# Kernel tuning notes

Hardware: AMD Instinct MI355X
Metric: run time of the kernel (lower is better)

The kernel has to match this reference:

```python
import jax, jax.numpy as jnp
import numpy as np

N = 8192      # active sparse voxels
C = 768       # model_channels
H = 12        # heads
DH = 64       # head dim
NB = 12       # blocks
WS = 8        # window size
RES = 64      # voxel grid resolution
NG = 32       # gaussians per voxel
OUT_CH = 448  # 96+96+96+128+32


def _radical_inverse(base, n):
    inv, f = 0.0, 1.0 / base
    while n > 0:
        inv += f * (n % base)
        n //= base
        f /= base
    return inv


def _hammersley(num):
    return np.array([[i / num, _radical_inverse(2, i), _radical_inverse(3, i)]
                     for i in range(num)], dtype=np.float32)


def _windows(coords, shift):
    # swin partition: window id of each voxel after shifting coords
    wc = (coords.astype(np.int64) + shift) // WS
    G = (RES + shift) // WS + 1
    wid = (wc[:, 0] * G + wc[:, 1]) * G + wc[:, 2]
    uniq, vwin, counts = np.unique(wid, return_inverse=True, return_counts=True)
    nw, cap, n = len(uniq), int(counts.max()), len(wid)
    order = np.argsort(wid, kind='stable')
    starts = np.concatenate([[0], np.cumsum(counts)[:-1]])
    slot_sorted = np.arange(n) - starts[vwin[order]]
    vslot = np.empty(n, dtype=np.int64)
    vslot[order] = slot_sorted
    idx = np.full((nw, cap), n, dtype=np.int32)  # n = padding row
    idx[vwin, vslot] = np.arange(n)
    mask = idx < n
    return (jnp.asarray(idx), jnp.asarray(mask),
            jnp.asarray(vwin.astype(np.int32)), jnp.asarray(vslot.astype(np.int32)))


def setup_inputs() -> dict:
    rng = np.random.RandomState(0)
    coords = rng.randint(0, RES, size=(N, 3)).astype(np.int32)
    feats = rng.randn(N, 8).astype(np.float32)
    idx0, mask0, vwin0, vslot0 = _windows(coords, 0)          # even blocks
    idx1, mask1, vwin1, vslot1 = _windows(coords, WS // 2)    # odd blocks (shifted)
    s = 0.02
    def w(*shape):
        return jnp.asarray((rng.randn(*shape) * s).astype(np.float32))
    perturb = _hammersley(NG) * 2.0 - 1.0
    perturb = np.arctanh(perturb / 1.5).astype(np.float32)  # voxel_size=1.5
    return dict(
        feats=jnp.asarray(feats), coords=jnp.asarray(coords),
        in_w=w(8, C), in_b=jnp.zeros((C,), jnp.float32),
        qkv_w=w(NB, C, 3 * C), qkv_b=jnp.zeros((NB, 3 * C), jnp.float32),
        proj_w=w(NB, C, C), proj_b=jnp.zeros((NB, C), jnp.float32),
        mlp_w1=w(NB, C, 4 * C), mlp_b1=jnp.zeros((NB, 4 * C), jnp.float32),
        mlp_w2=w(NB, 4 * C, C), mlp_b2=jnp.zeros((NB, C), jnp.float32),
        out_w=w(C, OUT_CH), out_b=jnp.zeros((OUT_CH,), jnp.float32),
        perturb=jnp.asarray(perturb),
        idx0=idx0, mask0=mask0, vwin0=vwin0, vslot0=vslot0,
        idx1=idx1, mask1=mask1, vwin1=vwin1, vslot1=vslot1,
    )


def _ln(x, eps):
    mu = jnp.mean(x, -1, keepdims=True)
    xc = x - mu
    var = jnp.mean(xc * xc, -1, keepdims=True)
    return xc * jax.lax.rsqrt(var + eps)


def _pos_embed(coords):
    freq_dim = C // 3 // 2  # 128
    freqs = 1.0 / (10000.0 ** (jnp.arange(freq_dim, dtype=jnp.float32) / freq_dim))
    phase = coords.astype(jnp.float32)[..., None] * freqs          # [N,3,128]
    emb = jnp.concatenate([jnp.sin(phase), jnp.cos(phase)], -1)    # [N,3,256]
    return emb.reshape(coords.shape[0], C)


def _win_attn(q, k, v, idx, mask):
    zpad = jnp.zeros((1,) + q.shape[1:], q.dtype)
    qw = jnp.concatenate([q, zpad], 0)[idx]   # [nw,cap,H,DH]
    kw = jnp.concatenate([k, zpad], 0)[idx]
    vw = jnp.concatenate([v, zpad], 0)[idx]
    scores = jnp.einsum('wihd,wjhd->whij', qw, kw) / np.float32(np.sqrt(DH))
    scores = jnp.where(mask[:, None, None, :], scores, jnp.float32(-1e9))
    attn = jax.nn.softmax(scores, axis=-1)
    return jnp.einsum('whij,wjhd->wihd', attn, vw)   # [nw,cap,H,DH]


def _forward(feats, coords, in_w, in_b, qkv_w, qkv_b, proj_w, proj_b,
             mlp_w1, mlp_b1, mlp_w2, mlp_b2, out_w, out_b, perturb,
             idx0, mask0, vwin0, vslot0, idx1, mask1, vwin1, vslot1):
    cfgs = [(idx0, mask0, vwin0, vslot0), (idx1, mask1, vwin1, vslot1)]
    n = feats.shape[0]
    h = feats @ in_w + in_b + _pos_embed(coords)
    for i in range(NB):
        idx, mask, vwin, vslot = cfgs[i % 2]
        qkv = (_ln(h, 1e-6) @ qkv_w[i] + qkv_b[i]).reshape(n, 3, H, DH)
        ow = _win_attn(qkv[:, 0], qkv[:, 1], qkv[:, 2], idx, mask)
        o = ow[vwin, vslot].reshape(n, C)
        h = h + (o @ proj_w[i] + proj_b[i])
        hid = jax.nn.gelu(_ln(h, 1e-6) @ mlp_w1[i] + mlp_b1[i], approximate=False)
        h = h + (hid @ mlp_w2[i] + mlp_b2[i])
    out = _ln(h, 1e-5) @ out_w + out_b   # F.layer_norm default eps
    # to_representation
    xyz = (coords.astype(jnp.float32) + 0.5) / RES                   # [N,3]
    off = out[:, :96].reshape(n, NG, 3)                               # lr=1.0
    off = jnp.tanh(off + perturb) / RES * 0.5 * 1.5                   # voxel_size=1.5
    g_xyz = (xyz[:, None, :] + off).reshape(n * NG, 3)
    g_dc = out[:, 96:192].reshape(n * NG, 3)
    g_scal = out[:, 192:288].reshape(n * NG, 3)
    g_rot = out[:, 288:416].reshape(n * NG, 4) * 0.1                  # lr=0.1
    g_opa = out[:, 416:448].reshape(n * NG, 1)
    return jnp.concatenate([g_xyz, g_dc, g_scal, g_rot, g_opa], -1)   # [N*32,14]


def reference(feats, coords, in_w, in_b, qkv_w, qkv_b, proj_w, proj_b,
              mlp_w1, mlp_b1, mlp_w2, mlp_b2, out_w, out_b, perturb,
              idx0, mask0, vwin0, vslot0, idx1, mask1, vwin1, vslot1):
    return _forward(feats, coords, in_w, in_b, qkv_w, qkv_b, proj_w, proj_b,
                    mlp_w1, mlp_b1, mlp_w2, mlp_b2, out_w, out_b, perturb,
                    idx0, mask0, vwin0, vslot0, idx1, mask1, vwin1, vslot1)
```

## Files before the change

### kernel.cpp

```cpp
#include <hip/hip_runtime.h>
#include <math.h>

#define NVOX 8192
#define CCH 768
#define NH 12
#define DH 64
#define NBLK 12
#define NG 32
#define OUT_CH 448
#define OUT_PAD 512
#define CAP 48
#define APITCH 72

typedef __attribute__((ext_vector_type(8))) short v8s;
typedef __attribute__((ext_vector_type(4))) float v4f;

__device__ __forceinline__ unsigned short f2bf(float f) {
  unsigned u = __builtin_bit_cast(unsigned, f);
  u += 0x7fffu + ((u >> 16) & 1u);
  return (unsigned short)(u >> 16);
}
__device__ __forceinline__ float bf2f(unsigned short b) {
  return __builtin_bit_cast(float, (unsigned)b << 16);
}

__device__ __forceinline__ void async16(const void* g, void* l) {
  __builtin_amdgcn_global_load_lds(
      (const __attribute__((address_space(1))) unsigned int*)g,
      (__attribute__((address_space(3))) unsigned int*)l, 16, 0, 0);
}

__global__ __launch_bounds__(256) void cap_kernel(const int* __restrict__ a,
                                                  const int* __restrict__ b,
                                                  int n, int* __restrict__ caps) {
  __shared__ int s0[256], s1[256];
  int m0 = 0, m1 = 0;
  for (int i = threadIdx.x; i < n; i += 256) {
    m0 = max(m0, a[i]);
    m1 = max(m1, b[i]);
  }
  s0[threadIdx.x] = m0;
  s1[threadIdx.x] = m1;
  __syncthreads();
  for (int st = 128; st > 0; st >>= 1) {
    if (threadIdx.x < st) {
      s0[threadIdx.x] = max(s0[threadIdx.x], s0[threadIdx.x + st]);
      s1[threadIdx.x] = max(s1[threadIdx.x], s1[threadIdx.x + st]);
    }
    __syncthreads();
  }
  if (threadIdx.x == 0) {
    caps[0] = s0[0] + 1;
    caps[1] = s1[0] + 1;
  }
}

__global__ __launch_bounds__(256) void embed_kernel(const float* __restrict__ feats,
                                                    const int* __restrict__ coords,
                                                    const float* __restrict__ in_w,
                                                    const float* __restrict__ in_b,
                                                    float* __restrict__ h) {
  int id = blockIdx.x * 256 + threadIdx.x;
  if (id >= NVOX * CCH) return;
  int n = id / CCH, c = id - n * CCH;
  float acc = in_b[c];
#pragma unroll
  for (int k = 0; k < 8; ++k) acc += feats[n * 8 + k] * in_w[k * CCH + c];
  int axis = c / 256;
  int r = c - axis * 256;
  int f = r & 127;
  float freq = __expf(-(float)f * (9.210340371976184f / 128.0f));
  float phase = (float)coords[n * 3 + axis] * freq;
  acc += (r < 128) ? __sinf(phase) : __cosf(phase);
  h[id] = acc;
}

__global__ __launch_bounds__(256) void ln_kernel(const float* __restrict__ x,
                                                 unsigned short* __restrict__ y,
                                                 float eps) {
  int row = blockIdx.x;
  const float* xr = x + (size_t)row * CCH;
  float v[3];
  float s = 0.f, s2 = 0.f;
#pragma unroll
  for (int j = 0; j < 3; ++j) {
    v[j] = xr[threadIdx.x + j * 256];
    s += v[j];
    s2 += v[j] * v[j];
  }
#pragma unroll
  for (int off = 32; off >= 1; off >>= 1) {
    s += __shfl_xor(s, off, 64);
    s2 += __shfl_xor(s2, off, 64);
  }
  __shared__ float ss[4], ss2[4];
  int wave = threadIdx.x >> 6, lane = threadIdx.x & 63;
  if (lane == 0) { ss[wave] = s; ss2[wave] = s2; }
  __syncthreads();
  s = ss[0] + ss[1] + ss[2] + ss[3];
  s2 = ss2[0] + ss2[1] + ss2[2] + ss2[3];
  float mu = s * (1.0f / CCH);
  float var = s2 * (1.0f / CCH) - mu * mu;
  float rr = rsqrtf(var + eps);
  unsigned short* yr = y + (size_t)row * CCH;
#pragma unroll
  for (int j = 0; j < 3; ++j) yr[threadIdx.x + j * 256] = f2bf((v[j] - mu) * rr);
}

__device__ __forceinline__ void wconv_tile(const float* __restrict__ W,
                                           unsigned short* __restrict__ Wt,
                                           int K, int Nsrc, int nt, int kt,
                                           float (*t)[65]) {
  int n0 = nt * 64, k0 = kt * 64;
  for (int e = threadIdx.x; e < 4096; e += 256) {
    int r = e >> 6, c = e & 63;
    int n = n0 + c;
    t[r][c] = (n < Nsrc) ? W[(size_t)(k0 + r) * Nsrc + n] : 0.f;
  }
  __syncthreads();
  for (int e = threadIdx.x; e < 4096; e += 256) {
    int rn = e >> 6, ck = e & 63;
    Wt[(size_t)(n0 + rn) * K + k0 + ck] = f2bf(t[ck][rn]);
  }
}

__global__ __launch_bounds__(256) void wconvert(const float* __restrict__ W,
                                                unsigned short* __restrict__ Wt,
                                                int K, int Nsrc) {
  __shared__ float t[64][65];
  wconv_tile(W, Wt, K, Nsrc, blockIdx.x, blockIdx.y, t);
}

__global__ __launch_bounds__(256) void wconvert4(const float* __restrict__ W0,
                                                 const float* __restrict__ W1,
                                                 const float* __restrict__ W2,
                                                 const float* __restrict__ W3,
                                                 unsigned short* __restrict__ D0,
                                                 unsigned short* __restrict__ D1,
                                                 unsigned short* __restrict__ D2,
                                                 unsigned short* __restrict__ D3) {
  __shared__ float t[64][65];
  int b = blockIdx.x;
  if (b < 432) {
    wconv_tile(W0, D0, 768, 2304, b / 12, b % 12, t);
  } else if (b < 576) {
    b -= 432;
    wconv_tile(W1, D1, 768, 768, b / 12, b % 12, t);
  } else if (b < 1152) {
    b -= 576;
    wconv_tile(W2, D2, 768, 3072, b / 12, b % 12, t);
  } else {
    b -= 1152;
    wconv_tile(W3, D3, 3072, 768, b / 48, b % 48, t);
  }
}

__device__ __forceinline__ float gelu_exact(float x) {
  return 0.5f * x * (1.0f + erff(x * 0.70710678118654752f));
}

template <int ACT, int RES, int OUTBF>
__global__ __launch_bounds__(256) void gemm_mfma(const unsigned short* __restrict__ A,
                                                 const unsigned short* __restrict__ Bt,
                                                 const float* __restrict__ bias, int Nbias,
                                                 float* __restrict__ outf,
                                                 unsigned short* __restrict__ outb,
                                                 int Nn, int K) {
  __shared__ __align__(16) unsigned short As[128 * 32];
  __shared__ __align__(16) unsigned short Bs[128 * 32];
  const int tid = threadIdx.x;
  const int lane = tid & 63, w = tid >> 6;
  const int row0 = blockIdx.y * 128, col0 = blockIdx.x * 128;
  const int wm = (w >> 1) * 64, wn = (w & 1) * 64;
  const int fm = lane & 15, fq = lane >> 4;

  const int c0 = w * 64 + lane;
  const int c1 = c0 + 256;
  const unsigned short* gA0 = A + (size_t)(row0 + (c0 >> 2)) * K + (c0 & 3) * 8;
  const unsigned short* gA1 = A + (size_t)(row0 + (c1 >> 2)) * K + (c1 & 3) * 8;
  const unsigned short* gB0 = Bt + (size_t)(col0 + (c0 >> 2)) * K + (c0 & 3) * 8;
  const unsigned short* gB1 = Bt + (size_t)(col0 + (c1 >> 2)) * K + (c1 & 3) * 8;
  unsigned short* lA0 = As + (size_t)(w * 64) * 8;
  unsigned short* lA1 = As + (size_t)(w * 64 + 256) * 8;
  unsigned short* lB0 = Bs + (size_t)(w * 64) * 8;
  unsigned short* lB1 = Bs + (size_t)(w * 64 + 256) * 8;

  v4f acc[4][4];
#pragma unroll
  for (int i = 0; i < 4; ++i)
#pragma unroll
    for (int j = 0; j < 4; ++j) acc[i][j] = (v4f){0.f, 0.f, 0.f, 0.f};

  for (int k0 = 0; k0 < K; k0 += 32) {
    async16(gA0 + k0, lA0);
    async16(gA1 + k0, lA1);
    async16(gB0 + k0, lB0);
    async16(gB1 + k0, lB1);
    __syncthreads();
    v8s af[4], bf[4];
#pragma unroll
    for (int i = 0; i < 4; ++i)
      af[i] = *(const v8s*)(As + (size_t)(wm + i * 16 + fm) * 32 + fq * 8);
#pragma unroll
    for (int j = 0; j < 4; ++j)
      bf[j] = *(const v8s*)(Bs + (size_t)(wn + j * 16 + fm) * 32 + fq * 8);
#pragma unroll
    for (int i = 0; i < 4; ++i)
#pragma unroll
      for (int j = 0; j < 4; ++j)
        acc[i][j] = __builtin_amdgcn_mfma_f32_16x16x32_bf16(af[i], bf[j], acc[i][j], 0, 0, 0);
    __syncthreads();
  }

#pragma unroll
  for (int i = 0; i < 4; ++i) {
    int row = row0 + wm + i * 16 + fq * 4;
#pragma unroll
    for (int j = 0; j < 4; ++j) {
      int col = col0 + wn + j * 16 + fm;
      float b = (col < Nbias) ? bias[col] : 0.f;
#pragma unroll
      for (int r = 0; r < 4; ++r) {
        float v = acc[i][j][r] + b;
        if (ACT == 1) v = gelu_exact(v);
        size_t o = (size_t)(row + r) * Nn + col;
        if (RES) {
          outf[o] += v;
        } else if (OUTBF) {
          outb[o] = f2bf(v);
        } else {
          outf[o] = v;
        }
      }
    }
  }
}

__global__ __launch_bounds__(64) void attn_kernel(const unsigned short* __restrict__ qkv,
                                                  const int* __restrict__ idx,
                                                  const int* __restrict__ capPtr,
                                                  int total,
                                                  unsigned short* __restrict__ attn_out) {
  __shared__ __align__(16) unsigned short QP[CAP * APITCH];
  __shared__ __align__(16) unsigned short Ks[CAP * APITCH];
  __shared__ __align__(16) unsigned short Vt[64 * APITCH];
  __shared__ int vox_lds[64];
  const int cap = *capPtr;
  if (cap > CAP) return;
  const int nw = total / cap;
  const int tasks = nw * NH;
  const int lane = threadIdx.x;
  const int fm = lane & 15, fq = lane >> 4;
  const v8s z8 = {0, 0, 0, 0, 0, 0, 0, 0};

  for (int task = blockIdx.x; task < tasks; task += gridDim.x) {
    const int w = task / NH, hh = task - w * NH;
    int vox_i = NVOX;
    if (lane < cap) vox_i = idx[w * cap + lane];
    vox_lds[lane] = vox_i;
    __syncthreads();

#pragma unroll
    for (int it = 0; it < 6; ++it) {
      int id = it * 64 + lane;
      int j = id >> 3, c = id & 7;
      int vj = vox_lds[j];
      v8s q8 = z8, k8 = z8;
      if (vj < NVOX) {
        const unsigned short* base = qkv + (size_t)vj * (3 * CCH) + hh * DH + c * 8;
        q8 = *(const v8s*)(base);
        k8 = *(const v8s*)(base + CCH);
      }
      *(v8s*)(QP + j * APITCH + c * 8) = q8;
      *(v8s*)(Ks + j * APITCH + c * 8) = k8;
    }
#pragma unroll 4
    for (int j = 0; j < CAP; ++j) {
      int vj = vox_lds[j];
      unsigned short vv = 0;
      if (vj < NVOX) vv = qkv[(size_t)vj * (3 * CCH) + 2 * CCH + hh * DH + lane];
      Vt[lane * APITCH + j] = vv;
    }
#pragma unroll
    for (int j = CAP; j < 64; ++j) Vt[lane * APITCH + j] = 0;
    __syncthreads();

    v4f s_acc[3][3];
#pragma unroll
    for (int mi = 0; mi < 3; ++mi)
#pragma unroll
      for (int jt = 0; jt < 3; ++jt) s_acc[mi][jt] = (v4f){0.f, 0.f, 0.f, 0.f};
#pragma unroll
    for (int ks = 0; ks < 2; ++ks) {
      v8s qf[3], kf[3];
#pragma unroll
      for (int mi = 0; mi < 3; ++mi)
        qf[mi] = *(const v8s*)(QP + (mi * 16 + fm) * APITCH + ks * 32 + fq * 8);
#pragma unroll
      for (int jt = 0; jt < 3; ++jt)
        kf[jt] = *(const v8s*)(Ks + (jt * 16 + fm) * APITCH + ks * 32 + fq * 8);
#pragma unroll
      for (int mi = 0; mi < 3; ++mi)
#pragma unroll
        for (int jt = 0; jt < 3; ++jt)
          s_acc[mi][jt] = __builtin_amdgcn_mfma_f32_16x16x32_bf16(qf[mi], kf[jt], s_acc[mi][jt], 0, 0, 0);
    }
    __syncthreads();

    bool va0 = (fm < cap) && (vox_lds[fm] < NVOX);
    bool va1 = (16 + fm < cap) && (vox_lds[16 + fm] < NVOX);
    bool va2 = (32 + fm < cap) && (vox_lds[32 + fm] < NVOX);
#pragma unroll
    for (int mi = 0; mi < 3; ++mi) {
#pragma unroll
      for (int r = 0; r < 4; ++r) {
        float e0 = va0 ? __expf(s_acc[mi][0][r] * 0.125f) : 0.f;
        float e1 = va1 ? __expf(s_acc[mi][1][r] * 0.125f) : 0.f;
        float e2 = va2 ? __expf(s_acc[mi][2][r] * 0.125f) : 0.f;
        float den = e0 + e1 + e2;
        den += __shfl_xor(den, 1, 64);
        den += __shfl_xor(den, 2, 64);
        den += __shfl_xor(den, 4, 64);
        den += __shfl_xor(den, 8, 64);
        float rden = (den > 0.f) ? 1.0f / den : 0.f;
        int row = mi * 16 + fq * 4 + r;
        QP[row * APITCH + fm] = f2bf(e0 * rden);
        QP[row * APITCH + 16 + fm] = f2bf(e1 * rden);
        QP[row * APITCH + 32 + fm] = f2bf(e2 * rden);
      }
    }
    if (lane < CAP) {
      *(v8s*)(QP + lane * APITCH + 48) = z8;
      *(v8s*)(QP + lane * APITCH + 56) = z8;
    }
    __syncthreads();

    v4f o_acc[3][4];
#pragma unroll
    for (int mi = 0; mi < 3; ++mi)
#pragma unroll
      for (int nt = 0; nt < 4; ++nt) o_acc[mi][nt] = (v4f){0.f, 0.f, 0.f, 0.f};
#pragma unroll
    for (int ks = 0; ks < 2; ++ks) {
      v8s pf[3], vf[4];
#pragma unroll
      for (int mi = 0; mi < 3; ++mi)
        pf[mi] = *(const v8s*)(QP + (mi * 16 + fm) * APITCH + ks * 32 + fq * 8);
#pragma unroll
      for (int nt = 0; nt < 4; ++nt)
        vf[nt] = *(const v8s*)(Vt + (nt * 16 + fm) * APITCH + ks * 32 + fq * 8);
#pragma unroll
      for (int mi = 0; mi < 3; ++mi)
#pragma unroll
        for (int nt = 0; nt < 4; ++nt)
          o_acc[mi][nt] = __builtin_amdgcn_mfma_f32_16x16x32_bf16(pf[mi], vf[nt], o_acc[mi][nt], 0, 0, 0);
    }

#pragma unroll
    for (int mi = 0; mi < 3; ++mi) {
#pragma unroll
      for (int r = 0; r < 4; ++r) {
        int i = mi * 16 + fq * 4 + r;
        int vox = vox_lds[i];
        if (i < cap && vox < NVOX) {
          unsigned short* ob = attn_out + (size_t)vox * CCH + hh * DH + fm;
#pragma unroll
          for (int nt = 0; nt < 4; ++nt) ob[nt * 16] = f2bf(o_acc[mi][nt][r]);
        }
      }
    }
    __syncthreads();
  }
}

__global__ __launch_bounds__(256) void decode_kernel(const float* __restrict__ outpad,
                                                     const int* __restrict__ coords,
                                                     const float* __restrict__ perturb,
                                                     float* __restrict__ out) {
  __shared__ float row[OUT_CH];
  const int n = blockIdx.x;
  const float* src = outpad + (size_t)n * OUT_PAD;
  for (int e = threadIdx.x; e < OUT_CH; e += 256) row[e] = src[e];
  __syncthreads();
  float* o = out + (size_t)n * OUT_CH;
  for (int e = threadIdx.x; e < OUT_CH; e += 256) {
    int g = e / 14, j = e - g * 14;
    float v;
    if (j < 3) {
      float xyz = ((float)coords[n * 3 + j] + 0.5f) * (1.0f / 64.0f);
      v = xyz + tanhf(row[g * 3 + j] + perturb[g * 3 + j]) * (0.75f / 64.0f);
    } else if (j < 6) {
      v = row[96 + g * 3 + (j - 3)];
    } else if (j < 9) {
      v = row[192 + g * 3 + (j - 6)];
    } else if (j < 13) {
      v = row[288 + g * 4 + (j - 9)] * 0.1f;
    } else {
      v = row[416 + g];
    }
    o[e] = v;
  }
}

extern "C" void kernel_launch(void* const* d_in, const int* in_sizes, int n_in,
                              void* d_out, int out_size, void* d_ws, size_t ws_size,
                              hipStream_t stream) {
  const float* feats = (const float*)d_in[0];
  const int* coords = (const int*)d_in[1];
  const float* in_w = (const float*)d_in[2];
  const float* in_b = (const float*)d_in[3];
  const float* qkv_w = (const float*)d_in[4];
  const float* qkv_b = (const float*)d_in[5];
  const float* proj_w = (const float*)d_in[6];
  const float* proj_b = (const float*)d_in[7];
  const float* mlp_w1 = (const float*)d_in[8];
  const float* mlp_b1 = (const float*)d_in[9];
  const float* mlp_w2 = (const float*)d_in[10];
  const float* mlp_b2 = (const float*)d_in[11];
  const float* out_w = (const float*)d_in[12];
  const float* out_b = (const float*)d_in[13];
  const float* perturb = (const float*)d_in[14];
  const int* idx0 = (const int*)d_in[15];
  const int* vslot0 = (const int*)d_in[18];
  const int* idx1 = (const int*)d_in[19];
  const int* vslot1 = (const int*)d_in[22];
  const int total0 = in_sizes[15];
  const int total1 = in_sizes[19];

  char* p = (char*)d_ws;
  int* caps = (int*)p;
  float* h = (float*)(p + 256);
  unsigned short* abuf = (unsigned short*)(p + 256 + 25165824);
  unsigned short* big = (unsigned short*)(p + 256 + 37748736);
  unsigned short* wst = (unsigned short*)(p + 256 + 88080384);
  float* outpad = (float*)(p + 256 + 102236160);
  const size_t OQ = 0;
  const size_t OP = (size_t)768 * 2304;
  const size_t OM1 = OP + (size_t)768 * 768;
  const size_t OM2 = OM1 + (size_t)768 * 3072;

  cap_kernel<<<1, 256, 0, stream>>>(vslot0, vslot1, NVOX, caps);
  embed_kernel<<<(NVOX * CCH + 255) / 256, 256, 0, stream>>>(feats, coords, in_w, in_b, h);

  for (int i = 0; i < NBLK; ++i) {
    const int* idx = (i & 1) ? idx1 : idx0;
    const int* capP = (i & 1) ? caps + 1 : caps;
    const int total = (i & 1) ? total1 : total0;

    wconvert4<<<1728, 256, 0, stream>>>(
        qkv_w + (size_t)i * 768 * 2304, proj_w + (size_t)i * 768 * 768,
        mlp_w1 + (size_t)i * 768 * 3072, mlp_w2 + (size_t)i * 3072 * 768,
        wst + OQ, wst + OP, wst + OM1, wst + OM2);

    ln_kernel<<<NVOX, 256, 0, stream>>>(h, abuf, 1e-6f);
    gemm_mfma<0, 0, 1><<<dim3(18, 64), 256, 0, stream>>>(
        abuf, wst + OQ, qkv_b + (size_t)i * 2304, 2304, nullptr, big, 2304, 768);
    attn_kernel<<<4096, 64, 0, stream>>>(big, idx, capP, total, abuf);
    gemm_mfma<0, 1, 0><<<dim3(6, 64), 256, 0, stream>>>(
        abuf, wst + OP, proj_b + (size_t)i * 768, 768, h, nullptr, 768, 768);
    ln_kernel<<<NVOX, 256, 0, stream>>>(h, abuf, 1e-6f);
    gemm_mfma<1, 0, 1><<<dim3(24, 64), 256, 0, stream>>>(
        abuf, wst + OM1, mlp_b1 + (size_t)i * 3072, 3072, nullptr, big, 3072, 768);
    gemm_mfma<0, 1, 0><<<dim3(6, 64), 256, 0, stream>>>(
        big, wst + OM2, mlp_b2 + (size_t)i * 768, 768, h, nullptr, 768, 3072);
  }

  ln_kernel<<<NVOX, 256, 0, stream>>>(h, abuf, 1e-5f);
  wconvert<<<dim3(8, 12), 256, 0, stream>>>(out_w, wst + OQ, 768, OUT_CH);
  gemm_mfma<0, 0, 0><<<dim3(4, 64), 256, 0, stream>>>(
      abuf, wst + OQ, out_b, OUT_CH, outpad, nullptr, OUT_PAD, 768);
  decode_kernel<<<NVOX, 256, 0, stream>>>(outpad, coords, perturb, (float*)d_out);
}
```

Before: 4.529 ms.

## Add split-K with atomic residual adds and XCD-aware block remapping to GEMMs

Adds a SPLITK template parameter so the residual-add GEMMs (proj with K=768, MLP down with K=3072) are split across 2 and 4 z-slices. Each slice accumulates its partial result into the fp32 residual with atomicAdd, and only slice 0 adds the bias. This raises the block count from 384 for these narrow-output GEMMs to fill the CUs. It also remaps workgroup ids so consecutive tiles land on the same XCD, aiming at better L2 reuse. The costs are atomic traffic and a summation order that is no longer deterministic.

```diff
diff --git a/kernel.cpp b/kernel.cpp
--- a/kernel.cpp
+++ b/kernel.cpp
@@ -159,7 +159,7 @@
   return 0.5f * x * (1.0f + erff(x * 0.70710678118654752f));
 }
 
-template <int ACT, int RES, int OUTBF>
+template <int ACT, int RES, int OUTBF, int SPLITK>
 __global__ __launch_bounds__(256) void gemm_mfma(const unsigned short* __restrict__ A,
                                                  const unsigned short* __restrict__ Bt,
                                                  const float* __restrict__ bias, int Nbias,
@@ -170,9 +170,25 @@
   __shared__ __align__(16) unsigned short Bs[128 * 32];
   const int tid = threadIdx.x;
   const int lane = tid & 63, w = tid >> 6;
-  const int row0 = blockIdx.y * 128, col0 = blockIdx.x * 128;
+
+  int bx = blockIdx.x, by = blockIdx.y;
+  {
+    const int gx = gridDim.x, gy = gridDim.y;
+    const int nwg = gx * gy;
+    const int id = by * gx + bx;
+    const int q = nwg >> 3, r = nwg & 7;
+    const int xc = id & 7, off = id >> 3;
+    const int nid = (xc < r ? xc * (q + 1) : r * (q + 1) + (xc - r) * q) + off;
+    bx = nid % gx;
+    by = nid / gx;
+  }
+  const int row0 = by * 128, col0 = bx * 128;
   const int wm = (w >> 1) * 64, wn = (w & 1) * 64;
   const int fm = lane & 15, fq = lane >> 4;
+
+  const int kz = (SPLITK > 1) ? blockIdx.z : 0;
+  const int Keff = K / SPLITK;
+  const int kbase = kz * Keff;
 
   const int c0 = w * 64 + lane;
   const int c1 = c0 + 256;
@@ -191,7 +207,7 @@
 #pragma unroll
     for (int j = 0; j < 4; ++j) acc[i][j] = (v4f){0.f, 0.f, 0.f, 0.f};
 
-  for (int k0 = 0; k0 < K; k0 += 32) {
+  for (int k0 = kbase; k0 < kbase + Keff; k0 += 32) {
     async16(gA0 + k0, lA0);
     async16(gA1 + k0, lA1);
     async16(gB0 + k0, lB0);
@@ -219,13 +235,18 @@
     for (int j = 0; j < 4; ++j) {
       int col = col0 + wn + j * 16 + fm;
       float b = (col < Nbias) ? bias[col] : 0.f;
+      if (SPLITK > 1 && kz != 0) b = 0.f;
 #pragma unroll
       for (int r = 0; r < 4; ++r) {
         float v = acc[i][j][r] + b;
         if (ACT == 1) v = gelu_exact(v);
         size_t o = (size_t)(row + r) * Nn + col;
         if (RES) {
-          outf[o] += v;
+          if (SPLITK > 1) {
+            atomicAdd(outf + o, v);
+          } else {
+            outf[o] += v;
+          }
         } else if (OUTBF) {
           outb[o] = f2bf(v);
         } else {
@@ -453,21 +474,21 @@
         wst + OQ, wst + OP, wst + OM1, wst + OM2);
 
     ln_kernel<<<NVOX, 256, 0, stream>>>(h, abuf, 1e-6f);
-    gemm_mfma<0, 0, 1><<<dim3(18, 64), 256, 0, stream>>>(
+    gemm_mfma<0, 0, 1, 1><<<dim3(18, 64), 256, 0, stream>>>(
         abuf, wst + OQ, qkv_b + (size_t)i * 2304, 2304, nullptr, big, 2304, 768);
     attn_kernel<<<4096, 64, 0, stream>>>(big, idx, capP, total, abuf);
-    gemm_mfma<0, 1, 0><<<dim3(6, 64), 256, 0, stream>>>(
+    gemm_mfma<0, 1, 0, 2><<<dim3(6, 64, 2), 256, 0, stream>>>(
         abuf, wst + OP, proj_b + (size_t)i * 768, 768, h, nullptr, 768, 768);
     ln_kernel<<<NVOX, 256, 0, stream>>>(h, abuf, 1e-6f);
-    gemm_mfma<1, 0, 1><<<dim3(24, 64), 256, 0, stream>>>(
+    gemm_mfma<1, 0, 1, 1><<<dim3(24, 64), 256, 0, stream>>>(
         abuf, wst + OM1, mlp_b1 + (size_t)i * 3072, 3072, nullptr, big, 3072, 768);
-    gemm_mfma<0, 1, 0><<<dim3(6, 64), 256, 0, stream>>>(
+    gemm_mfma<0, 1, 0, 4><<<dim3(6, 64, 4), 256, 0, stream>>>(
         big, wst + OM2, mlp_b2 + (size_t)i * 768, 768, h, nullptr, 768, 3072);
   }
 
   ln_kernel<<<NVOX, 256, 0, stream>>>(h, abuf, 1e-5f);
   wconvert<<<dim3(8, 12), 256, 0, stream>>>(out_w, wst + OQ, 768, OUT_CH);
-  gemm_mfma<0, 0, 0><<<dim3(4, 64), 256, 0, stream>>>(
+  gemm_mfma<0, 0, 0, 1><<<dim3(4, 64), 256, 0, stream>>>(
       abuf, wst + OQ, out_b, OUT_CH, outpad, nullptr, OUT_PAD, 768);
   decode_kernel<<<NVOX, 256, 0, stream>>>(outpad, coords, perturb, (float*)d_out);
 }
```

Result: slower. 4.851 ms (+7.1%).

## Double-buffer GEMM shared tiles and remap workgroups across XCDs

Applied to the files above, without the earlier changes.

Adds two-stage LDS double buffering to the MFMA GEMM: the next K-slice is loaded asynchronously while MFMAs run on the current one, cutting the barriers per iteration from two to one. It also remaps block IDs so consecutive tiles land on the same XCD chiplet, which is meant to improve L2 reuse. LDS use doubles to 32KB per block, which may reduce occupancy.

```diff
diff --git a/kernel.cpp b/kernel.cpp
--- a/kernel.cpp
+++ b/kernel.cpp
@@ -166,11 +166,23 @@
                                                  float* __restrict__ outf,
                                                  unsigned short* __restrict__ outb,
                                                  int Nn, int K) {
-  __shared__ __align__(16) unsigned short As[128 * 32];
-  __shared__ __align__(16) unsigned short Bs[128 * 32];
+  __shared__ __align__(16) unsigned short As[2][128 * 32];
+  __shared__ __align__(16) unsigned short Bs[2][128 * 32];
   const int tid = threadIdx.x;
   const int lane = tid & 63, w = tid >> 6;
-  const int row0 = blockIdx.y * 128, col0 = blockIdx.x * 128;
+
+  int bx = blockIdx.x, by = blockIdx.y;
+  {
+    const int gx = gridDim.x, gy = gridDim.y;
+    const int nwg = gx * gy;
+    const int id = by * gx + bx;
+    const int q = nwg >> 3, r = nwg & 7;
+    const int xc = id & 7, off = id >> 3;
+    const int nid = (xc < r ? xc * (q + 1) : r * (q + 1) + (xc - r) * q) + off;
+    bx = nid % gx;
+    by = nid / gx;
+  }
+  const int row0 = by * 128, col0 = bx * 128;
   const int wm = (w >> 1) * 64, wn = (w & 1) * 64;
   const int fm = lane & 15, fq = lane >> 4;
 
@@ -180,10 +192,8 @@
   const unsigned short* gA1 = A + (size_t)(row0 + (c1 >> 2)) * K + (c1 & 3) * 8;
   const unsigned short* gB0 = Bt + (size_t)(col0 + (c0 >> 2)) * K + (c0 & 3) * 8;
   const unsigned short* gB1 = Bt + (size_t)(col0 + (c1 >> 2)) * K + (c1 & 3) * 8;
-  unsigned short* lA0 = As + (size_t)(w * 64) * 8;
-  unsigned short* lA1 = As + (size_t)(w * 64 + 256) * 8;
-  unsigned short* lB0 = Bs + (size_t)(w * 64) * 8;
-  unsigned short* lB1 = Bs + (size_t)(w * 64 + 256) * 8;
+  const int oL0 = w * 512;
+  const int oL1 = w * 512 + 2048;
 
   v4f acc[4][4];
 #pragma unroll
@@ -191,25 +201,47 @@
 #pragma unroll
     for (int j = 0; j < 4; ++j) acc[i][j] = (v4f){0.f, 0.f, 0.f, 0.f};
 
-  for (int k0 = 0; k0 < K; k0 += 32) {
-    async16(gA0 + k0, lA0);
-    async16(gA1 + k0, lA1);
-    async16(gB0 + k0, lB0);
-    async16(gB1 + k0, lB1);
-    __syncthreads();
-    v8s af[4], bf[4];
+  async16(gA0, As[0] + oL0);
+  async16(gA1, As[0] + oL1);
+  async16(gB0, Bs[0] + oL0);
+  async16(gB1, Bs[0] + oL1);
+  __syncthreads();
+
+  int cur = 0;
+  for (int k0 = 32; k0 < K; k0 += 32) {
+    const int nxt = cur ^ 1;
+    async16(gA0 + k0, As[nxt] + oL0);
+    async16(gA1 + k0, As[nxt] + oL1);
+    async16(gB0 + k0, Bs[nxt] + oL0);
+    async16(gB1 + k0, Bs[nxt] + oL1);
+    v8s af[4], bfv[4];
 #pragma unroll
     for (int i = 0; i < 4; ++i)
-      af[i] = *(const v8s*)(As + (size_t)(wm + i * 16 + fm) * 32 + fq * 8);
+      af[i] = *(const v8s*)(As[cur] + (wm + i * 16 + fm) * 32 + fq * 8);
 #pragma unroll
     for (int j = 0; j < 4; ++j)
-      bf[j] = *(const v8s*)(Bs + (size_t)(wn + j * 16 + fm) * 32 + fq * 8);
+      bfv[j] = *(const v8s*)(Bs[cur] + (wn + j * 16 + fm) * 32 + fq * 8);
 #pragma unroll
     for (int i = 0; i < 4; ++i)
 #pragma unroll
       for (int j = 0; j < 4; ++j)
-        acc[i][j] = __builtin_amdgcn_mfma_f32_16x16x32_bf16(af[i], bf[j], acc[i][j], 0, 0, 0);
-    __syncthreads();
+        acc[i][j] = __builtin_amdgcn_mfma_f32_16x16x32_bf16(af[i], bfv[j], acc[i][j], 0, 0, 0);
+    __syncthreads();
+    cur = nxt;
+  }
+  {
+    v8s af[4], bfv[4];
+#pragma unroll
+    for (int i = 0; i < 4; ++i)
+      af[i] = *(const v8s*)(As[cur] + (wm + i * 16 + fm) * 32 + fq * 8);
+#pragma unroll
+    for (int j = 0; j < 4; ++j)
+      bfv[j] = *(const v8s*)(Bs[cur] + (wn + j * 16 + fm) * 32 + fq * 8);
+#pragma unroll
+    for (int i = 0; i < 4; ++i)
+#pragma unroll
+      for (int j = 0; j < 4; ++j)
+        acc[i][j] = __builtin_amdgcn_mfma_f32_16x16x32_bf16(af[i], bfv[j], acc[i][j], 0, 0, 0);
   }
 
 #pragma unroll
```

Result: faster. 4.400 ms (-2.8%).
